# Performance work log

Measured on AMD Instinct MI355X. Metric: run time of the kernel, lower is better.

The kernel has to match this reference:

```python
import jax, jax.numpy as jnp
import numpy as np

T, P, H, W = 100, 2, 120, 160
BS = 8
HB, WB = H // BS, W // BS          # 15, 20
NB = HB * WB                        # 300 blocks
D = 4096                            # out_features (HD dimension)


def _rand_pm1(key, shape):
    # torchhd Random embedding: random bipolar (+1/-1) hypervectors
    return jnp.where(jax.random.bernoulli(key, 0.5, shape), 1.0, -1.0).astype(jnp.float32)


def setup_inputs() -> dict:
    key = jax.random.key(0)
    k0, k1, k2, k3, k4 = jax.random.split(key, 5)
    x = jax.random.uniform(k0, (T, P, H, W), dtype=jnp.float32)  # event frames
    proj_w = jax.random.normal(k1, (D,), dtype=jnp.float32)      # Projection(1, D) weight [D,1] -> [D]
    pos_hv = _rand_pm1(k2, (NB, D))
    pol_hv = _rand_pm1(k3, (P, D))
    time_hv = _rand_pm1(k4, (T, D))   # T <= max_time_bins=100, no clamp needed
    return {"x": x, "proj_w": proj_w, "pos_hv": pos_hv, "pol_hv": pol_hv, "time_hv": time_hv}


def reference(x, proj_w, pos_hv, pol_hv, time_hv):
    t, p, h, w = x.shape
    hb, wb = h // BS, w // BS
    # per-block event counts: [T, P, NB]  (equivalent to F.unfold + sum)
    counts = x.reshape(t, p, hb, BS, wb, BS).sum(axis=(3, 5)).reshape(t, p, hb * wb)
    # RAFE: scalar count -> projection -> sin activation: [T, P, NB, D]
    act = jnp.sin(counts[..., None] * proj_w)
    # bind (elementwise multiply in MAP) with position, polarity, time HVs,
    # then multiset bundle (sum over t, p, blocks). Zero frames contribute 0
    # automatically since sin(0)=0, matching the skip branch in the original.
    bundled = jnp.einsum('tpnd,nd,pd,td->d', act, pos_hv, pol_hv, time_hv)
    # torchhd.normalize for MAP: hard quantize to sign
    return jnp.sign(bundled)
```

## Files before the change

kernel.cpp:

```cpp
#include <hip/hip_runtime.h>
#include <hip/hip_bf16.h>


#define T_ 100
#define P_ 2
#define H_ 120
#define W_ 160
#define BS_ 8
#define WB_ 20
#define NB_ 300
#define D_ 4096
#define NR_ 25
#define TCB_ 10
#define GY_ 125

typedef float f32x2 __attribute__((ext_vector_type(2)));

static __device__ __forceinline__ f32x2 splat(float v) {
    f32x2 r; r.x = v; r.y = v; return r;
}

__global__ __launch_bounds__(256) void k_counts(const float* __restrict__ x,
                                                float* __restrict__ cq) {
    int idx = blockIdx.x * 256 + threadIdx.x;
    if (idx >= T_ * P_ * NB_) return;
    int n  = idx % NB_;
    int tp = idx / NB_;
    int p  = tp & 1;
    int t  = tp >> 1;
    int hb = n / WB_;
    int wb = n % WB_;
    const float* base = x + ((size_t)tp * H_ + hb * BS_) * W_ + wb * BS_;
    float s = 0.f;
#pragma unroll
    for (int i = 0; i < BS_; ++i) {
        const float4* row = reinterpret_cast<const float4*>(base + i * W_);
        float4 a = row[0];
        float4 b = row[1];
        s += a.x + a.y + a.z + a.w + b.x + b.y + b.z + b.w;
    }
    cq[(((size_t)(t >> 1) * NB_ + n) << 2) + (t & 1) * 2 + p] = s;
}

__global__ __launch_bounds__(256) void k_encode(const float4* __restrict__ cq,
                                                const float* __restrict__ proj_w,
                                                const float* __restrict__ pos_hv,
                                                const float* __restrict__ pol_hv,
                                                const float* __restrict__ time_hv,
                                                float* __restrict__ partial) {
    const int d   = blockIdx.x * 256 + threadIdx.x;
    const int y   = blockIdx.y;
    const int tcg = y / NR_;
    const int nr  = y - tcg * NR_;
    const int n0  = nr * 12;
    const int tc0 = tcg * TCB_;
    const int t0  = tc0 * 2;

    const unsigned SGN = 0x80000000u;
    const unsigned uw  = __float_as_uint(proj_w[d] * 0.15915494309189535f);

    float pf[12];
#pragma unroll
    for (int j = 0; j < 12; ++j)
        pf[j] = pos_hv[(size_t)(n0 + j) * D_ + d];

    f32x2 accA = {0.f, 0.f};
    f32x2 accB = {0.f, 0.f};

    const float4* cb = cq + (size_t)tc0 * NB_ + n0;
    const float*  th = time_hv + (size_t)t0 * D_ + d;

#pragma unroll 2
    for (int k = 0; k < TCB_; ++k) {
        const unsigned sa = __float_as_uint(th[(size_t)(2 * k) * D_])     & SGN;
        const unsigned sb = __float_as_uint(th[(size_t)(2 * k + 1) * D_]) & SGN;
        const f32x2 wA = splat(__uint_as_float(uw ^ sa));
        const f32x2 wB = splat(__uint_as_float(uw ^ sb));
        const float4* ck = cb + (size_t)k * NB_;
#pragma unroll
        for (int j = 0; j < 12; j += 2) {
            float4 cj0 = ck[j];
            float4 cj1 = ck[j + 1];
            f32x2 a01; a01.x = cj0.x; a01.y = cj0.y;
            f32x2 a23; a23.x = cj0.z; a23.y = cj0.w;
            f32x2 b01; b01.x = cj1.x; b01.y = cj1.y;
            f32x2 b23; b23.x = cj1.z; b23.y = cj1.w;

            f32x2 pa0 = a01 * wA;
            f32x2 pa1 = a23 * wB;
            f32x2 pb0 = b01 * wA;
            f32x2 pb1 = b23 * wB;

            f32x2 s1, s2, s3, s4;
            s1.x = __builtin_amdgcn_sinf(pa0.x);
            s1.y = __builtin_amdgcn_sinf(pa0.y);
            s2.x = __builtin_amdgcn_sinf(pa1.x);
            s2.y = __builtin_amdgcn_sinf(pa1.y);
            s3.x = __builtin_amdgcn_sinf(pb0.x);
            s3.y = __builtin_amdgcn_sinf(pb0.y);
            s4.x = __builtin_amdgcn_sinf(pb1.x);
            s4.y = __builtin_amdgcn_sinf(pb1.y);

            const f32x2 g0 = splat(pf[j]);
            const f32x2 g1 = splat(pf[j + 1]);
            accA += s1 * g0;
            accB += s2 * g0;
            accA += s3 * g1;
            accB += s4 * g1;
        }
    }

    const float pol0 = pol_hv[d];
    const float pol1 = pol_hv[D_ + d];
    partial[(size_t)y * D_ + d] =
        (accA.x + accB.x) * pol0 + (accA.y + accB.y) * pol1;
}

__global__ __launch_bounds__(320) void k_reduce(const float* __restrict__ partial,
                                                float* __restrict__ out) {
    __shared__ float red[5][64];
    const int lane = threadIdx.x;
    const int w    = threadIdx.y;
    const int d    = blockIdx.x * 64 + lane;
    float a = 0.f;
#pragma unroll
    for (int i = 0; i < GY_ / 5; ++i)
        a += partial[(size_t)(w * (GY_ / 5) + i) * D_ + d];
    red[w][lane] = a;
    __syncthreads();
    if (w == 0) {
        float s = ((red[0][lane] + red[1][lane]) + (red[2][lane] + red[3][lane]))
                  + red[4][lane];
        out[d] = (s > 0.f) ? 1.f : ((s < 0.f) ? -1.f : 0.f);
    }
}

extern "C" void kernel_launch(void* const* d_in, const int* in_sizes, int n_in,
                              void* d_out, int out_size, void* d_ws, size_t ws_size,
                              hipStream_t stream) {
    const float* x       = (const float*)d_in[0];
    const float* proj_w  = (const float*)d_in[1];
    const float* pos_hv  = (const float*)d_in[2];
    const float* pol_hv  = (const float*)d_in[3];
    const float* time_hv = (const float*)d_in[4];
    float* out = (float*)d_out;

    float* counts_q = (float*)d_ws;
    float* partial  = (float*)((char*)d_ws + (256u << 10));

    {
        int total = T_ * P_ * NB_;
        k_counts<<<dim3((total + 255) / 256), dim3(256), 0, stream>>>(x, counts_q);
    }
    k_encode<<<dim3(16, GY_), dim3(256), 0, stream>>>(
        (const float4*)counts_q, proj_w, pos_hv, pol_hv, time_hv, partial);
    k_reduce<<<dim3(D_ / 64), dim3(64, 5), 0, stream>>>(partial, out);
}
```

Measured before the change: 39.11 us.

## Split block-count reduction across 8 threads and prefetch time signs

The counts kernel now uses eight threads per 8x8 block, one per row, and combines the row sums with wave shuffles. This raises parallelism and improves coalescing on the 15 MB input read, which is likely the dominant memory cost. The encode kernel also software-prefetches the next iteration's time-hypervector sign bits to hide load latency. The cost is 8x more threads in the counts kernel and a few extra registers in encode.

```diff
diff --git a/kernel.cpp b/kernel.cpp
--- a/kernel.cpp
+++ b/kernel.cpp
@@ -8,6 +8,7 @@
 #define W_ 160
 #define BS_ 8
 #define WB_ 20
+#define HB_ 15
 #define NB_ 300
 #define D_ 4096
 #define NR_ 25
@@ -22,24 +23,33 @@
 
 __global__ __launch_bounds__(256) void k_counts(const float* __restrict__ x,
                                                 float* __restrict__ cq) {
-    int idx = blockIdx.x * 256 + threadIdx.x;
-    if (idx >= T_ * P_ * NB_) return;
-    int n  = idx % NB_;
-    int tp = idx / NB_;
-    int p  = tp & 1;
-    int t  = tp >> 1;
-    int hb = n / WB_;
-    int wb = n % WB_;
-    const float* base = x + ((size_t)tp * H_ + hb * BS_) * W_ + wb * BS_;
-    float s = 0.f;
-#pragma unroll
-    for (int i = 0; i < BS_; ++i) {
-        const float4* row = reinterpret_cast<const float4*>(base + i * W_);
-        float4 a = row[0];
-        float4 b = row[1];
-        s += a.x + a.y + a.z + a.w + b.x + b.y + b.z + b.w;
+    int gid  = blockIdx.x * 256 + threadIdx.x;
+    int cell = gid >> 3;
+    int row  = gid & 7;
+
+    int wb = cell % WB_;
+    int r1 = cell / WB_;
+    int hb = r1 % HB_;
+    int tp = r1 / HB_;
+
+    const float4* rp = reinterpret_cast<const float4*>(
+        x + ((size_t)tp * H_ + hb * BS_ + row) * W_ + wb * BS_);
+    float4 a = rp[0];
+    float4 b = rp[1];
+    float s = (a.x + a.y + a.z + a.w) + (b.x + b.y + b.z + b.w);
+
+    s += __shfl_xor(s, 1, 64);
+    s += __shfl_xor(s, 2, 64);
+    s += __shfl_xor(s, 4, 64);
+
+    if (row == 0) {
+        int t  = tp >> 1;
+        int p  = tp & 1;
+        int n  = hb * WB_ + wb;
+        int tc = t >> 1;
+        int tl = t & 1;
+        cq[(((size_t)tc * NB_ + n) << 2) + tl * 2 + p] = s;
     }
-    cq[(((size_t)(t >> 1) * NB_ + n) << 2) + (t & 1) * 2 + p] = s;
 }
 
 __global__ __launch_bounds__(256) void k_encode(const float4* __restrict__ cq,
@@ -70,10 +80,16 @@
     const float4* cb = cq + (size_t)tc0 * NB_ + n0;
     const float*  th = time_hv + (size_t)t0 * D_ + d;
 
+    unsigned sa = __float_as_uint(th[0])          & SGN;
+    unsigned sb = __float_as_uint(th[(size_t)D_]) & SGN;
+
 #pragma unroll 2
     for (int k = 0; k < TCB_; ++k) {
-        const unsigned sa = __float_as_uint(th[(size_t)(2 * k) * D_])     & SGN;
-        const unsigned sb = __float_as_uint(th[(size_t)(2 * k + 1) * D_]) & SGN;
+        unsigned nsa = 0u, nsb = 0u;
+        if (k + 1 < TCB_) {
+            nsa = __float_as_uint(th[(size_t)(2 * k + 2) * D_]) & SGN;
+            nsb = __float_as_uint(th[(size_t)(2 * k + 3) * D_]) & SGN;
+        }
         const f32x2 wA = splat(__uint_as_float(uw ^ sa));
         const f32x2 wB = splat(__uint_as_float(uw ^ sb));
         const float4* ck = cb + (size_t)k * NB_;
@@ -108,6 +124,8 @@
             accA += s3 * g1;
             accB += s4 * g1;
         }
+        sa = nsa;
+        sb = nsb;
     }
 
     const float pol0 = pol_hv[d];
@@ -148,10 +166,8 @@
     float* counts_q = (float*)d_ws;
     float* partial  = (float*)((char*)d_ws + (256u << 10));
 
-    {
-        int total = T_ * P_ * NB_;
-        k_counts<<<dim3((total + 255) / 256), dim3(256), 0, stream>>>(x, counts_q);
-    }
+    k_counts<<<dim3(1875), dim3(256), 0, stream>>>(x, counts_q);
+
     k_encode<<<dim3(16, GY_), dim3(256), 0, stream>>>(
         (const float4*)counts_q, proj_w, pos_hv, pol_hv, time_hv, partial);
     k_reduce<<<dim3(D_ / 64), dim3(64, 5), 0, stream>>>(partial, out);
```

After: 37.96 us. 2.9% less time.
